# Kernel optimization log

Measured on AMD Instinct MI355X. Metric: run time of the kernel, lower is better.

## Reference

```python
import jax, jax.numpy as jnp
import numpy as np
from jax import lax
from jax.scipy.special import logsumexp

TRIGGER_SIZE = 34
NTAG = TRIGGER_SIZE + 2  # +START/STOP
START = TRIGGER_SIZE
STOP = TRIGGER_SIZE + 1


def setup_inputs() -> dict:
    key = jax.random.key(0)
    k1, k2, k3, k4, k5 = jax.random.split(key, 5)
    B, S, H = 64, 512, 768
    x_1 = jax.random.normal(k1, (B, S, H), dtype=jnp.float32)
    head_indexes = jax.random.randint(k2, (B, S), 0, S)
    triggers_y = jax.random.randint(k3, (B, S), 0, TRIGGER_SIZE)
    W = jax.random.normal(k4, (H, NTAG), dtype=jnp.float32) * (1.0 / np.sqrt(H))
    b = jnp.zeros((NTAG,), dtype=jnp.float32)
    transitions = jax.random.normal(k5, (NTAG, NTAG), dtype=jnp.float32) * 0.1
    return {"x_1": x_1, "head_indexes": head_indexes, "triggers_y": triggers_y,
            "W": W, "b": b, "transitions": transitions}


def crf_nll(emit, mask, tags, trans):
    # emit [B,S,T], mask [B,S] bool, tags [B,S], trans [T,T] (from->to)
    B, S, T = emit.shape
    maskf = mask.astype(emit.dtype)
    # --- partition (forward algorithm) ---
    alpha0 = emit[:, 0] + trans[START][None, :]  # [B,T]; pos 0 always valid

    def fstep(alpha, inp):
        e_t, m_t = inp  # [B,T], [B]
        new = logsumexp(alpha[:, :, None] + trans[None, :, :], axis=1) + e_t
        return jnp.where(m_t[:, None], new, alpha), None

    alpha, _ = lax.scan(fstep, alpha0,
                        (emit[:, 1:].transpose(1, 0, 2), mask[:, 1:].T))
    logZ = logsumexp(alpha + trans[:, STOP][None, :], axis=1)  # [B]
    # --- gold path score ---
    emit_g = jnp.take_along_axis(emit, tags[:, :, None], axis=2)[..., 0]  # [B,S]
    emit_score = (emit_g * maskf).sum(axis=1)
    trans_pair = trans[tags[:, :-1], tags[:, 1:]]  # [B,S-1]
    trans_score = (trans_pair * maskf[:, 1:]).sum(axis=1)
    xlen = mask.sum(axis=1)  # [B]
    last_tag = jnp.take_along_axis(tags, (xlen - 1)[:, None], axis=1)[:, 0]
    gold = emit_score + trans[START, tags[:, 0]] + trans_score + trans[last_tag, STOP]
    return jnp.sum(logZ - gold)


def crf_viterbi(emit, mask, trans):
    B, S, T = emit.shape
    ids = jnp.arange(T)
    delta0 = emit[:, 0] + trans[START][None, :]

    def vstep(delta, inp):
        e_t, m_t = inp
        scores = delta[:, :, None] + trans[None, :, :]  # [B,T,T]
        best = scores.max(axis=1) + e_t
        bp = jnp.argmax(scores, axis=1)  # [B,T]
        new_delta = jnp.where(m_t[:, None], best, delta)
        bp = jnp.where(m_t[:, None], bp, ids[None, :])  # identity on pad
        return new_delta, bp

    delta, bps = lax.scan(vstep, delta0,
                          (emit[:, 1:].transpose(1, 0, 2), mask[:, 1:].T))
    final = delta + trans[:, STOP][None, :]
    last_tag = jnp.argmax(final, axis=1)  # [B]
    path_score = jnp.max(final, axis=1)

    def back(tag_next, bp_t):
        tag_t = jnp.take_along_axis(bp_t, tag_next[:, None], axis=1)[:, 0]
        return tag_t, tag_t

    _, prev_tags = lax.scan(back, last_tag, bps, reverse=True)  # [S-1,B]
    path = jnp.concatenate([prev_tags.T, last_tag[:, None]], axis=1)  # [B,S]
    path = jnp.where(mask, path, 0)
    return path_score, path


def reference(x_1, head_indexes, triggers_y, W, b, transitions):
    B, S, H = x_1.shape
    # batched version of the per-sample index_select loop
    x = jnp.take_along_axis(x_1, head_indexes[:, :, None], axis=1)  # [B,S,H]
    xlen = head_indexes.max(axis=1)  # xlen = [max(row) for row in head_indexes]
    mask = jnp.arange(S)[None, :] < xlen[:, None]  # [B,S] bool
    logits = jax.nn.leaky_relu(x @ W + b)  # tri_fc1 + leaky_relu (dropout=eval)
    trigger_loss = crf_nll(logits, mask, triggers_y, transitions)
    path_score, trigger_hat = crf_viterbi(logits, mask, transitions)
    return trigger_loss, trigger_hat, path_score
```

## Files before the change

kernel.cpp:

```cpp
#include <hip/hip_runtime.h>
#include <math.h>

#define SB 64
#define SS 512
#define SH 768
#define NT 36
#define TSTART 34
#define TSTOP 35
#define NC 32
#define CL 16
#define APAD 40

#define CFENCE() asm volatile("" ::: "memory")

__device__ __forceinline__ float wave_max_f(float v) {
#pragma unroll
    for (int off = 32; off > 0; off >>= 1) v = fmaxf(v, __shfl_xor(v, off, 64));
    return v;
}
__device__ __forceinline__ float wave_sum_f(float v) {
#pragma unroll
    for (int off = 32; off > 0; off >>= 1) v += __shfl_xor(v, off, 64);
    return v;
}
__device__ __forceinline__ float bcast0(float v) {
    return __uint_as_float(__builtin_amdgcn_readfirstlane(__float_as_uint(v)));
}

#define DOT4(pv, k4)                                                     \
    {                                                                    \
        const float* wr = Wq + (size_t)((k4) * 4) * NT;                  \
        _Pragma("unroll")                                                \
        for (int j = 0; j < NT; ++j) acc[j] += (pv).x * wr[j];           \
        _Pragma("unroll")                                                \
        for (int j = 0; j < NT; ++j) acc[j] += (pv).y * wr[NT + j];      \
        _Pragma("unroll")                                                \
        for (int j = 0; j < NT; ++j) acc[j] += (pv).z * wr[2 * NT + j];  \
        _Pragma("unroll")                                                \
        for (int j = 0; j < NT; ++j) acc[j] += (pv).w * wr[3 * NT + j];  \
    }

extern "C" __global__ __launch_bounds__(512, 4) void k_emit(
    const float* __restrict__ x1, const int* __restrict__ hidx,
    const float* __restrict__ W, const float* __restrict__ bias,
    float* __restrict__ emit)
{
    __shared__ __align__(16) float red[4][64][37];

    int tid  = threadIdx.x;
    int lane = tid & 63;
    int q    = __builtin_amdgcn_readfirstlane(tid >> 6);
    int gr   = blockIdx.x * 64 + lane;
    int b    = gr >> 9;
    const float4* xr = (const float4*)(x1 + (size_t)(b * SS + hidx[gr]) * SH) + q * 24;
    const float*  Wq = W + (size_t)q * 96 * NT;

    float acc[NT];
#pragma unroll
    for (int j = 0; j < NT; ++j) acc[j] = 0.f;

    float4 p0 = xr[0], p1 = xr[1], p2 = xr[2], p3 = xr[3];
    float4 p4 = xr[4], p5 = xr[5], p6 = xr[6], p7 = xr[7];
    for (int kb = 0; kb < 16; kb += 8) {
        float4 n0 = xr[kb + 8],  n1 = xr[kb + 9];
        float4 n2 = xr[kb + 10], n3 = xr[kb + 11];
        float4 n4 = xr[kb + 12], n5 = xr[kb + 13];
        float4 n6 = xr[kb + 14], n7 = xr[kb + 15];
        DOT4(p0, kb);     DOT4(p1, kb + 1);
        DOT4(p2, kb + 2); DOT4(p3, kb + 3);
        DOT4(p4, kb + 4); DOT4(p5, kb + 5);
        DOT4(p6, kb + 6); DOT4(p7, kb + 7);
        p0 = n0; p1 = n1; p2 = n2; p3 = n3;
        p4 = n4; p5 = n5; p6 = n6; p7 = n7;
    }
    DOT4(p0, 16); DOT4(p1, 17); DOT4(p2, 18); DOT4(p3, 19);
    DOT4(p4, 20); DOT4(p5, 21); DOT4(p6, 22); DOT4(p7, 23);

    if (q >= 4) {
#pragma unroll
        for (int j = 0; j < NT; ++j) red[q - 4][lane][j] = acc[j];
    }
    __syncthreads();
    if (q < 4) {
#pragma unroll
        for (int j = 0; j < NT; ++j) acc[j] += red[q][lane][j];
    }
    __syncthreads();
    if (q == 2 || q == 3) {
#pragma unroll
        for (int j = 0; j < NT; ++j) red[q - 2][lane][j] = acc[j];
    }
    __syncthreads();
    if (q < 2) {
#pragma unroll
        for (int j = 0; j < NT; ++j) acc[j] += red[q][lane][j];
    }
    __syncthreads();
    if (q == 1) {
#pragma unroll
        for (int j = 0; j < NT; ++j) red[1][lane][j] = acc[j];
    }
    __syncthreads();
    if (q == 0) {
        alignas(16) float vout[NT];
#pragma unroll
        for (int j = 0; j < NT; ++j) {
            float v = acc[j] + red[1][lane][j] + bias[j];
            vout[j] = v > 0.f ? v : 0.01f * v;
        }
        float4* op = (float4*)(emit + (size_t)gr * NT);
        const float4* vv = (const float4*)vout;
#pragma unroll
        for (int i = 0; i < 9; ++i) op[i] = vv[i];
    }
}

extern "C" __global__ __launch_bounds__(256) void k_scan(
    const float* __restrict__ emit, const int* __restrict__ hidx,
    const float* __restrict__ trans,
    float* __restrict__ A0,
    float* __restrict__ delta_ws, float* __restrict__ lse_local,
    float* __restrict__ score_local, int* __restrict__ ltag,
    unsigned char* __restrict__ bp, int pass)
{
    __shared__ float trl[NT * NT];
    __shared__ float els[4][768];
    __shared__ float4 bc4[4][16];

    int tid  = threadIdx.x;
    int lane = tid & 63;
    int w    = __builtin_amdgcn_readfirstlane(tid >> 6);

    int wid  = blockIdx.x * 4 + w;
    int kind = wid >> 11;
    int rem  = wid & 2047;
    int b    = rem >> 5;
    int c    = rem & 31;

    const float* eb    = emit + (size_t)b * SS * NT;
    const float* ebase = eb + (size_t)c * CL * NT;
    float* elsw = els[w];

#pragma unroll
    for (int i = 0; i < 3; ++i) {
        __builtin_amdgcn_global_load_lds(
            (const __attribute__((address_space(1))) void*)(ebase + i * 256 + lane * 4),
            (__attribute__((address_space(3))) void*)(elsw + i * 256), 16, 0, 0);
    }
    for (int i = tid; i < NT * NT; i += 256) trl[i] = trans[i];

    int  jj  = lane < NT ? lane : NT - 1;
    bool act = lane < NT;

    int xm = 0;
    const int* hb = hidx + b * SS;
#pragma unroll
    for (int k = 0; k < SS / 64; ++k) xm = max(xm, hb[lane + 64 * k]);
#pragma unroll
    for (int off = 32; off > 0; off >>= 1) xm = max(xm, __shfl_xor(xm, off, 64));
    int xlen = xm;
    int cl   = (xlen >= 1) ? ((xlen - 1) >> 4) : 0;

    int tb = (pass == 0) ? (c * CL + 8) : (c * CL);
    if (tb < 1) tb = 1;
    int te = (c + 1) * CL; if (te > xlen) te = xlen; te -= 1;

    size_t aoff = (size_t)((((kind << 6) | b) << 5) | c) * APAD;
    int didx = (kind * SB + b) * NC + c;

    float alpha;
    if (pass == 0)      alpha = act ? eb[(tb - 1) * NT + jj] : -1e30f;
    else if (c == 0)    alpha = act ? (eb[jj] + trans[TSTART * NT + jj]) : -1e30f;
    else                alpha = act ? A0[aoff - APAD + jj] : -1e30f;

    float a0prev = (pass == 1) ? A0[aoff] : 0.f;

    __syncthreads();

    float* bc = (float*)bc4[w];
    int t0 = c * CL;

    if (kind == 0) {
        float Ecol[NT];
#pragma unroll
        for (int i = 0; i < NT; ++i) Ecol[i] = __expf(trl[i * NT + jj]);
        for (int t = tb; t <= te; ++t) {
            float e_t = elsw[(t - t0) * NT + jj];
            float m = bcast0(alpha);
            float p = __expf(alpha - m);
            bc[lane] = p;
            CFENCE();
            __builtin_amdgcn_wave_barrier();
            float s0 = 0.f, s1 = 0.f, s2 = 0.f, s3 = 0.f;
#pragma unroll
            for (int k = 0; k < 9; ++k) {
                float4 pv = bc4[w][k];
                s0 += pv.x * Ecol[4 * k];
                s1 += pv.y * Ecol[4 * k + 1];
                s2 += pv.z * Ecol[4 * k + 2];
                s3 += pv.w * Ecol[4 * k + 3];
            }
            CFENCE();
            float anew = m + __logf((s0 + s1) + (s2 + s3)) + e_t;
            alpha = act ? anew : -1e30f;
        }
        if (pass == 0) {
            if (act) A0[aoff + jj] = alpha;
        } else {
            float a0r = bcast0(a0prev);
            if (lane == 0) delta_ws[didx] = alpha - a0r;
            if (c == cl) {
                float ff = act ? (alpha + trl[jj * NT + TSTOP]) : -1e30f;
                float M = wave_max_f(ff);
                float ssum = wave_sum_f(__expf(ff - M));
                if (lane == 0) lse_local[b] = M + __logf(ssum);
            }
        }
    } else {
        float tcol[NT];
#pragma unroll
        for (int i = 0; i < NT; ++i) tcol[i] = trl[i * NT + jj];
        for (int t = tb; t <= te; ++t) {
            float e_t = elsw[(t - t0) * NT + jj];
            bc[lane] = alpha;
            CFENCE();
            __builtin_amdgcn_wave_barrier();
            float b0 = -1e30f, b1 = -1e30f, b2 = -1e30f, b3 = -1e30f;
            int   i0 = 0, i1 = 1, i2 = 2, i3 = 3;
#pragma unroll
            for (int k = 0; k < 9; ++k) {
                float4 dv = bc4[w][k];
                float c0 = dv.x + tcol[4 * k];
                float c1 = dv.y + tcol[4 * k + 1];
                float c2 = dv.z + tcol[4 * k + 2];
                float c3 = dv.w + tcol[4 * k + 3];
                if (c0 > b0) { b0 = c0; i0 = 4 * k; }
                if (c1 > b1) { b1 = c1; i1 = 4 * k + 1; }
                if (c2 > b2) { b2 = c2; i2 = 4 * k + 2; }
                if (c3 > b3) { b3 = c3; i3 = 4 * k + 3; }
            }
            CFENCE();
            float best = b0; int bi = i0;
            if (b1 > best || (b1 == best && i1 < bi)) { best = b1; bi = i1; }
            if (b2 > best || (b2 == best && i2 < bi)) { best = b2; bi = i2; }
            if (b3 > best || (b3 == best && i3 < bi)) { best = b3; bi = i3; }
            float dnew = best + e_t;
            alpha = act ? dnew : -1e30f;
            if (pass == 1 && act) bp[((size_t)b * SS + t) * 64 + jj] = (unsigned char)bi;
        }
        if (pass == 0) {
            if (act) A0[aoff + jj] = alpha;
        } else {
            float a0r = bcast0(a0prev);
            if (lane == 0) delta_ws[didx] = alpha - a0r;
            if (c == cl) {
                float ff = act ? (alpha + trl[jj * NT + TSTOP]) : -1e30f;
                float bv = ff; int bi = lane;
#pragma unroll
                for (int off = 32; off > 0; off >>= 1) {
                    float ov = __shfl_xor(bv, off, 64);
                    int   oi = __shfl_xor(bi, off, 64);
                    if (ov > bv || (ov == bv && oi < bi)) { bv = ov; bi = oi; }
                }
                if (lane == 0) { score_local[b] = bv; ltag[b] = bi; }
            }
        }
    }
}

extern "C" __global__ __launch_bounds__(1024) void k_final(
    const float* __restrict__ emit, const int* __restrict__ hidx,
    const int* __restrict__ tags, const float* __restrict__ trans,
    const float* __restrict__ delta_ws, const float* __restrict__ lse_local,
    const float* __restrict__ score_local, const int* __restrict__ ltag,
    const unsigned char* __restrict__ bp,
    float* __restrict__ loss_out, float* __restrict__ path_out,
    float* __restrict__ score_out)
{
    __shared__ unsigned char bpl[SS * 64];
    __shared__ unsigned char cmap[SS][40];
    __shared__ unsigned char exitmap[NC][64];
    __shared__ float gred[16];
    __shared__ int   ent[NC];

    int tid  = threadIdx.x;
    int lane = tid & 63;
    int w    = tid >> 6;
    int b    = blockIdx.x;

    {
        const int4* src = (const int4*)(bp + (size_t)b * SS * 64);
        int4* dst = (int4*)bpl;
        for (int i = tid; i < SS * 4; i += 1024) dst[i] = src[i];
    }

    int xm = 0;
    const int* hb = hidx + b * SS;
#pragma unroll
    for (int k = 0; k < SS / 64; ++k) xm = max(xm, hb[lane + 64 * k]);
#pragma unroll
    for (int off = 32; off > 0; off >>= 1) xm = max(xm, __shfl_xor(xm, off, 64));
    int xlen = xm;
    int cl   = (xlen >= 1) ? ((xlen - 1) >> 4) : 0;

    float g = 0.f;
    const int* tg = tags + b * SS;
    if (tid < SS) {
        int t = tid;
        if (t < xlen) {
            int tt = tg[t];
            g += emit[((size_t)b * SS + t) * NT + tt];
            if (t >= 1) g += trans[tg[t - 1] * NT + tt];
        }
    }
    g = wave_sum_f(g);
    if (lane == 0) gred[w] = g;

    float kf = 0.f, kv = 0.f;
    if (w == 8) {
        if (lane < cl) {
            kf = delta_ws[(0 * SB + b) * NC + lane];
            kv = delta_ws[(1 * SB + b) * NC + lane];
        }
        kf = wave_sum_f(kf);
        kv = wave_sum_f(kv);
    }

    __syncthreads();

    if (tid == 512) {
        float gold = 0.f;
#pragma unroll
        for (int i = 0; i < 8; ++i) gold += gred[i];
        int tg0 = tg[0];
        int lt  = (xlen >= 1) ? tg[xlen - 1] : tg0;
        gold += trans[TSTART * NT + tg0] + trans[lt * NT + TSTOP];
        atomicAdd(loss_out, (lse_local[b] + kf) - gold);
        score_out[b] = score_local[b] + kv;
    }

    for (int cc = 0; cc < 2; ++cc) {
        int c = w * 2 + cc;
        if (xlen >= 1 && c <= cl) {
            int tb = (c == 0) ? 1 : c * CL;
            int te = c * CL + CL - 1; if (te > xlen - 1) te = xlen - 1;
            int m = lane;
            if (lane < NT) cmap[te][lane] = (unsigned char)m;
            for (int t = te; t >= tb; --t) {
                m = bpl[t * 64 + m];
                if (lane < NT) {
                    if (t > tb || c == 0) cmap[t - 1][lane] = (unsigned char)m;
                    else                  exitmap[c][lane]  = (unsigned char)m;
                }
            }
        }
    }
    __syncthreads();

    if (tid == 0 && xlen >= 1) {
        int e = ltag[b];
        for (int c2 = cl; c2 >= 0; --c2) {
            ent[c2] = e;
            if (c2 > 0) e = exitmap[c2][e];
        }
    }
    __syncthreads();

    if (tid < SS) {
        int t = tid;
        float* op = path_out + (size_t)b * SS;
        if (t >= xlen) op[t] = 0.f;
        else           op[t] = (float)cmap[t][ent[t >> 4]];
    }
}

extern "C" void kernel_launch(void* const* d_in, const int* in_sizes, int n_in,
                              void* d_out, int out_size, void* d_ws, size_t ws_size,
                              hipStream_t stream)
{
    const float* x1    = (const float*)d_in[0];
    const int*   hidx  = (const int*)d_in[1];
    const int*   tags  = (const int*)d_in[2];
    const float* W     = (const float*)d_in[3];
    const float* bias  = (const float*)d_in[4];
    const float* trans = (const float*)d_in[5];
    float* out = (float*)d_out;

    float* emit        = (float*)d_ws;
    float* A0          = emit + (size_t)SB * SS * NT;
    float* delta_ws    = A0 + 2 * SB * NC * APAD;
    float* lse_local   = delta_ws + 2 * SB * NC;
    float* score_local = lse_local + SB;
    int*   ltag        = (int*)(score_local + SB);
    float* lossp       = (float*)(ltag + SB);
    unsigned char* bp  = (unsigned char*)(lossp + SB);

    hipLaunchKernelGGL(k_emit, dim3(SB * SS / 64), dim3(512), 0, stream,
                       x1, hidx, W, bias, emit);
    hipLaunchKernelGGL(k_scan, dim3(1024), dim3(256), 0, stream,
                       emit, hidx, trans, A0, delta_ws, lse_local,
                       score_local, ltag, bp, 0);
    hipLaunchKernelGGL(k_scan, dim3(1024), dim3(256), 0, stream,
                       emit, hidx, trans, A0, delta_ws, lse_local,
                       score_local, ltag, bp, 1);
    hipLaunchKernelGGL(k_final, dim3(SB), dim3(1024), 0, stream,
                       emit, hidx, tags, trans, delta_ws, lse_local,
                       score_local, ltag, bp, out, out + 1, out + 1 + SB * SS);
}
```

Baseline: 212.2 us.

## Stage W in LDS and process 128 rows per 1024-thread emit block

The emission-projection kernel now copies the whole weight matrix W into shared memory at block start and reads weights from LDS instead of global memory. Blocks grow to 1024 threads covering two 64-row groups, so the W staging cost is shared across more rows. The cross-wave reduction tree is reworked to handle both row groups, and the x prefetch depth drops from 8 to 4 float4s. In exchange, every block pays for a ~110KB W copy, and the large LDS footprint limits each CU to one block, which may reduce latency hiding compared with the uniform weight loads used before.

```diff
diff --git a/kernel.cpp b/kernel.cpp
--- a/kernel.cpp
+++ b/kernel.cpp
@@ -29,7 +29,7 @@
 
 #define DOT4(pv, k4)                                                     \
     {                                                                    \
-        const float* wr = Wq + (size_t)((k4) * 4) * NT;                  \
+        const float* wr = Wl + (size_t)(q * 24 + (k4)) * 144;            \
         _Pragma("unroll")                                                \
         for (int j = 0; j < NT; ++j) acc[j] += (pv).x * wr[j];           \
         _Pragma("unroll")                                                \
@@ -40,72 +40,86 @@
         for (int j = 0; j < NT; ++j) acc[j] += (pv).w * wr[3 * NT + j];  \
     }
 
-extern "C" __global__ __launch_bounds__(512, 4) void k_emit(
+extern "C" __global__ __launch_bounds__(1024) void k_emit(
     const float* __restrict__ x1, const int* __restrict__ hidx,
     const float* __restrict__ W, const float* __restrict__ bias,
     float* __restrict__ emit)
 {
+    __shared__ __align__(16) float Wl[SH * NT];
     __shared__ __align__(16) float red[4][64][37];
 
     int tid  = threadIdx.x;
     int lane = tid & 63;
-    int q    = __builtin_amdgcn_readfirstlane(tid >> 6);
-    int gr   = blockIdx.x * 64 + lane;
-    int b    = gr >> 9;
+    int w    = __builtin_amdgcn_readfirstlane(tid >> 6);
+    int q    = w & 7;
+    int rg   = w >> 3;
+
+    {
+        const float4* Ws = (const float4*)W;
+        float4* Wd = (float4*)Wl;
+        for (int i = tid; i < SH * NT / 4; i += 1024) Wd[i] = Ws[i];
+    }
+
+    int gr = blockIdx.x * 128 + rg * 64 + lane;
+    int b  = gr >> 9;
     const float4* xr = (const float4*)(x1 + (size_t)(b * SS + hidx[gr]) * SH) + q * 24;
-    const float*  Wq = W + (size_t)q * 96 * NT;
 
     float acc[NT];
 #pragma unroll
     for (int j = 0; j < NT; ++j) acc[j] = 0.f;
 
     float4 p0 = xr[0], p1 = xr[1], p2 = xr[2], p3 = xr[3];
-    float4 p4 = xr[4], p5 = xr[5], p6 = xr[6], p7 = xr[7];
-    for (int kb = 0; kb < 16; kb += 8) {
-        float4 n0 = xr[kb + 8],  n1 = xr[kb + 9];
-        float4 n2 = xr[kb + 10], n3 = xr[kb + 11];
-        float4 n4 = xr[kb + 12], n5 = xr[kb + 13];
-        float4 n6 = xr[kb + 14], n7 = xr[kb + 15];
+    __syncthreads();
+
+    for (int kb = 0; kb < 20; kb += 4) {
+        float4 n0 = xr[kb + 4], n1 = xr[kb + 5];
+        float4 n2 = xr[kb + 6], n3 = xr[kb + 7];
         DOT4(p0, kb);     DOT4(p1, kb + 1);
         DOT4(p2, kb + 2); DOT4(p3, kb + 3);
-        DOT4(p4, kb + 4); DOT4(p5, kb + 5);
-        DOT4(p6, kb + 6); DOT4(p7, kb + 7);
         p0 = n0; p1 = n1; p2 = n2; p3 = n3;
-        p4 = n4; p5 = n5; p6 = n6; p7 = n7;
-    }
-    DOT4(p0, 16); DOT4(p1, 17); DOT4(p2, 18); DOT4(p3, 19);
-    DOT4(p4, 20); DOT4(p5, 21); DOT4(p6, 22); DOT4(p7, 23);
-
-    if (q >= 4) {
-#pragma unroll
-        for (int j = 0; j < NT; ++j) red[q - 4][lane][j] = acc[j];
-    }
-    __syncthreads();
-    if (q < 4) {
-#pragma unroll
-        for (int j = 0; j < NT; ++j) acc[j] += red[q][lane][j];
+    }
+    DOT4(p0, 20); DOT4(p1, 21); DOT4(p2, 22); DOT4(p3, 23);
+
+    if (q == 4 || q == 5) {
+#pragma unroll
+        for (int j = 0; j < NT; ++j) red[2 * rg + (q - 4)][lane][j] = acc[j];
+    }
+    __syncthreads();
+    if (q == 0 || q == 1) {
+#pragma unroll
+        for (int j = 0; j < NT; ++j) acc[j] += red[2 * rg + q][lane][j];
+    }
+    __syncthreads();
+    if (q == 6 || q == 7) {
+#pragma unroll
+        for (int j = 0; j < NT; ++j) red[2 * rg + (q - 6)][lane][j] = acc[j];
     }
     __syncthreads();
     if (q == 2 || q == 3) {
 #pragma unroll
-        for (int j = 0; j < NT; ++j) red[q - 2][lane][j] = acc[j];
-    }
-    __syncthreads();
-    if (q < 2) {
-#pragma unroll
-        for (int j = 0; j < NT; ++j) acc[j] += red[q][lane][j];
+        for (int j = 0; j < NT; ++j) acc[j] += red[2 * rg + (q - 2)][lane][j];
+    }
+    __syncthreads();
+    if (q == 2 || q == 3) {
+#pragma unroll
+        for (int j = 0; j < NT; ++j) red[2 * rg + (q - 2)][lane][j] = acc[j];
+    }
+    __syncthreads();
+    if (q == 0 || q == 1) {
+#pragma unroll
+        for (int j = 0; j < NT; ++j) acc[j] += red[2 * rg + q][lane][j];
     }
     __syncthreads();
     if (q == 1) {
 #pragma unroll
-        for (int j = 0; j < NT; ++j) red[1][lane][j] = acc[j];
+        for (int j = 0; j < NT; ++j) red[2 * rg][lane][j] = acc[j];
     }
     __syncthreads();
     if (q == 0) {
         alignas(16) float vout[NT];
 #pragma unroll
         for (int j = 0; j < NT; ++j) {
-            float v = acc[j] + red[1][lane][j] + bias[j];
+            float v = acc[j] + red[2 * rg][lane][j] + bias[j];
             vout[j] = v > 0.f ? v : 0.01f * v;
         }
         float4* op = (float4*)(emit + (size_t)gr * NT);
@@ -395,7 +409,7 @@
     float* lossp       = (float*)(ltag + SB);
     unsigned char* bp  = (unsigned char*)(lossp + SB);
 
-    hipLaunchKernelGGL(k_emit, dim3(SB * SS / 64), dim3(512), 0, stream,
+    hipLaunchKernelGGL(k_emit, dim3(SB * SS / 128), dim3(1024), 0, stream,
                        x1, hidx, W, bias, emit);
     hipLaunchKernelGGL(k_scan, dim3(1024), dim3(256), 0, stream,
                        emit, hidx, trans, A0, delta_ws, lse_local,
```

Result: no change. 211.6 us (-0.3%).
